# Kernel optimization log

Hardware: AMD Instinct MI355X
Metric: run time of the kernel (lower is better)

The kernel has to match this reference:

```python
import jax, jax.numpy as jnp
import numpy as np

N, B, E = 10000, 4, 160000
C_IN, C_OUT, C_E = 64, 64, 16


def _mk_params(key, c_in, c_out, c_e):
    ks = jax.random.split(key, 8)
    s = 0.1
    return dict(
        w_n=jax.random.normal(ks[0], (c_in, c_out), jnp.float32) * s,
        w_e=jax.random.normal(ks[1], (c_e, c_out), jnp.float32) * s,
        q=jax.random.normal(ks[2], (c_out, c_out), jnp.float32) * s,
        k=jax.random.normal(ks[3], (c_out, c_out), jnp.float32) * s,
        aw=jax.random.normal(ks[4], (3 * c_out, 1), jnp.float32) * s,
        ab=jax.random.normal(ks[5], (1,), jnp.float32) * s,
        ow=jax.random.normal(ks[6], (2 * c_out, c_out), jnp.float32) * s,
        ob=jax.random.normal(ks[7], (c_out,), jnp.float32) * s,
    )


def setup_inputs() -> dict:
    key = jax.random.key(0)
    kx, ke, ka, k1, k2 = jax.random.split(key, 5)
    inp = {
        'X': jax.random.normal(kx, (N, B, C_IN), jnp.float32),
        'edge_index': jax.random.randint(ke, (2, E), 0, N, jnp.int32),
        'edge_attr': jax.random.normal(ka, (E, C_E), jnp.float32),
    }
    p1 = _mk_params(k1, C_IN, C_OUT, C_E)
    p2 = _mk_params(k2, C_OUT, C_OUT, C_E)
    for name, v in p1.items():
        inp[name + '1'] = v
    for name, v in p2.items():
        inp[name + '2'] = v
    return inp


def egnn_conv(x, edge_index, edge_attr, w_n, w_e, q, k, aw, ab, ow, ob, n_nodes):
    # x: [N,B,Cin]; edge_attr: [E,Ce]
    xp = x @ w_n                         # [N,B,C]
    ea = edge_attr @ w_e                 # [E,C]
    src, dst = edge_index[0], edge_index[1]
    xj = xp[src]                         # [E,B,C] gather (source)
    xi = xp[dst]                         # [E,B,C] gather (target)
    qf = xj @ q                          # [E,B,C]
    kf = xi @ k                          # [E,B,C]
    eab = jnp.broadcast_to(ea[:, None, :], qf.shape)  # [E,B,C]
    att_feat = jnp.concatenate([qf, kf, eab], axis=-1)  # [E,B,3C]
    att = jax.nn.sigmoid(att_feat @ aw + ab)            # [E,B,1]
    gate = jax.nn.sigmoid(eab)
    msg = att * xj * gate                # [E,B,C]
    aggr = jax.ops.segment_max(msg, dst, num_segments=n_nodes)  # [N,B,C]
    aggr = jnp.where(jnp.isneginf(aggr), 0.0, aggr)  # empty segments -> 0
    out = jnp.concatenate([xp, aggr], axis=-1) @ ow + ob
    return xp + out


def reference(X, edge_index, edge_attr,
              w_n1, w_e1, q1, k1, aw1, ab1, ow1, ob1,
              w_n2, w_e2, q2, k2, aw2, ab2, ow2, ob2):
    n_nodes = X.shape[0]
    c1 = egnn_conv(X, edge_index, edge_attr, w_n1, w_e1, q1, k1, aw1, ab1, ow1, ob1, n_nodes)
    c1 = jax.nn.leaky_relu(c1, 0.01)
    c2 = egnn_conv(c1, edge_index, edge_attr, w_n2, w_e2, q2, k2, aw2, ab2, ow2, ob2, n_nodes)
    c2 = jax.nn.leaky_relu(c2, 0.01)
    return c2
```

## Files before the change

### kernel.cpp

```cpp
#include <hip/hip_runtime.h>
#include <math.h>

#define NN 10000
#define BB 4
#define EE 160000
#define CC 64
#define CE 16

static constexpr size_t OFF_XPA    = 0;
static constexpr size_t OFF_XPB    = 10240000;
static constexpr size_t OFF_SA     = 20480000;
static constexpr size_t OFF_SB     = 20640000;
static constexpr size_t OFF_VECS   = 20800000;
static constexpr size_t OFF_COUNTS = 20801280;
static constexpr size_t OFF_CURSOR = 20841280;
static constexpr size_t OFF_OFFS   = 20881280;
static constexpr size_t OFF_RECS   = 20921344;
static constexpr size_t OFF_ATT    = 22201344;
static constexpr size_t OFF_SE12   = 24761344;
static constexpr size_t OFF_ORDER  = 26041344;

__device__ __forceinline__ float sigmoidf_(float x) {
    return __builtin_amdgcn_rcpf(1.0f + __expf(-x));
}

__device__ __forceinline__ float bcast_(float v, int l) {
    return __uint_as_float(__builtin_amdgcn_readlane(__float_as_uint(v), l));
}

__global__ void hist_vecs_kernel(const int* __restrict__ ei, int* __restrict__ counts,
                                 const float* __restrict__ q1, const float* __restrict__ k1,
                                 const float* __restrict__ aw1, const float* __restrict__ we1,
                                 const float* __restrict__ q2, const float* __restrict__ k2,
                                 const float* __restrict__ aw2, const float* __restrict__ we2,
                                 float* __restrict__ vecs) {
    int e = blockIdx.x * blockDim.x + threadIdx.x;
    if (e < EE) atomicAdd(&counts[ei[EE + e]], 1);
    if (blockIdx.x == 0) {
        int t = threadIdx.x;
        if (t < 64) {
            float a = 0.f, b = 0.f, c = 0.f, d = 0.f;
            for (int j = 0; j < 64; ++j) {
                a = fmaf(q1[t * 64 + j], aw1[j], a);
                b = fmaf(k1[t * 64 + j], aw1[64 + j], b);
                c = fmaf(q2[t * 64 + j], aw2[j], c);
                d = fmaf(k2[t * 64 + j], aw2[64 + j], d);
            }
            vecs[t] = a; vecs[64 + t] = b; vecs[144 + t] = c; vecs[208 + t] = d;
        }
        if (t < 16) {
            float a = 0.f, b = 0.f;
            for (int j = 0; j < 64; ++j) {
                a = fmaf(we1[t * 64 + j], aw1[128 + j], a);
                b = fmaf(we2[t * 64 + j], aw2[128 + j], b);
            }
            vecs[128 + t] = a; vecs[272 + t] = b;
        }
    }
}

__global__ __launch_bounds__(1024) void scan_order_kernel(const int* __restrict__ counts,
                                                          int* __restrict__ offs,
                                                          int* __restrict__ order) {
    __shared__ int hist[1024];
    __shared__ int cur[1024];
    __shared__ int startb[1024];
    __shared__ int wsum[16];
    int t = threadIdx.x;
    hist[t] = 0; cur[t] = 0;
    int lane = t & 63, wid = t >> 6;
    int v[10];
    int s = 0;
    #pragma unroll
    for (int j = 0; j < 10; ++j) {
        int i = t * 10 + j;
        v[j] = (i < NN) ? counts[i] : 0;
        s += v[j];
    }
    int ps = s;
    #pragma unroll
    for (int off = 1; off < 64; off <<= 1) {
        int u = __shfl_up(ps, off, 64);
        if (lane >= off) ps += u;
    }
    if (lane == 63) wsum[wid] = ps;
    __syncthreads();
    int wbase = 0;
    for (int w = 0; w < wid; ++w) wbase += wsum[w];
    int tb = wbase + ps - s;
    #pragma unroll
    for (int j = 0; j < 10; ++j) {
        int i = t * 10 + j;
        if (i < NN) offs[i] = tb;
        tb += v[j];
    }
    if (t == 1023) offs[NN] = tb;
    #pragma unroll
    for (int j = 0; j < 10; ++j) {
        int i = t * 10 + j;
        if (i < NN) {
            int d = v[j] > 1023 ? 1023 : v[j];
            atomicAdd(&hist[d], 1);
        }
    }
    __syncthreads();
    int r = 1023 - t;
    int hv = hist[r];
    int ps2 = hv;
    #pragma unroll
    for (int off = 1; off < 64; off <<= 1) {
        int u = __shfl_up(ps2, off, 64);
        if (lane >= off) ps2 += u;
    }
    if (lane == 63) wsum[wid] = ps2;
    __syncthreads();
    int wb2 = 0;
    for (int w = 0; w < wid; ++w) wb2 += wsum[w];
    startb[r] = wb2 + ps2 - hv;
    __syncthreads();
    #pragma unroll
    for (int j = 0; j < 10; ++j) {
        int i = t * 10 + j;
        if (i < NN) {
            int d = v[j] > 1023 ? 1023 : v[j];
            int pos = startb[d] + atomicAdd(&cur[d], 1);
            order[pos] = i;
        }
    }
}

__global__ __launch_bounds__(256) void scatter_kernel(
    const int* __restrict__ ei, const int* __restrict__ offs,
    int* __restrict__ cursor, const float* __restrict__ attr,
    const float* __restrict__ vecs, const float* __restrict__ ab1,
    const float* __restrict__ ab2, int2* __restrict__ recs,
    float2* __restrict__ se12) {
    int e = blockIdx.x * blockDim.x + threadIdx.x;
    if (e >= EE) return;
    int s = ei[e], d = ei[EE + e];
    const float4* ap = (const float4*)(attr + (size_t)e * CE);
    float4 a0 = ap[0], a1 = ap[1], a2 = ap[2], a3 = ap[3];
    const float* v1 = vecs + 128;
    const float* v2 = vecs + 272;
    float s1 = ab1[0], s2 = ab2[0];
    s1 = fmaf(a0.x, v1[0], s1);  s1 = fmaf(a0.y, v1[1], s1);
    s1 = fmaf(a0.z, v1[2], s1);  s1 = fmaf(a0.w, v1[3], s1);
    s1 = fmaf(a1.x, v1[4], s1);  s1 = fmaf(a1.y, v1[5], s1);
    s1 = fmaf(a1.z, v1[6], s1);  s1 = fmaf(a1.w, v1[7], s1);
    s1 = fmaf(a2.x, v1[8], s1);  s1 = fmaf(a2.y, v1[9], s1);
    s1 = fmaf(a2.z, v1[10], s1); s1 = fmaf(a2.w, v1[11], s1);
    s1 = fmaf(a3.x, v1[12], s1); s1 = fmaf(a3.y, v1[13], s1);
    s1 = fmaf(a3.z, v1[14], s1); s1 = fmaf(a3.w, v1[15], s1);
    s2 = fmaf(a0.x, v2[0], s2);  s2 = fmaf(a0.y, v2[1], s2);
    s2 = fmaf(a0.z, v2[2], s2);  s2 = fmaf(a0.w, v2[3], s2);
    s2 = fmaf(a1.x, v2[4], s2);  s2 = fmaf(a1.y, v2[5], s2);
    s2 = fmaf(a1.z, v2[6], s2);  s2 = fmaf(a1.w, v2[7], s2);
    s2 = fmaf(a2.x, v2[8], s2);  s2 = fmaf(a2.y, v2[9], s2);
    s2 = fmaf(a2.z, v2[10], s2); s2 = fmaf(a2.w, v2[11], s2);
    s2 = fmaf(a3.x, v2[12], s2); s2 = fmaf(a3.y, v2[13], s2);
    s2 = fmaf(a3.z, v2[14], s2); s2 = fmaf(a3.w, v2[15], s2);
    int p = atomicAdd(&cursor[d], 1);
    recs[offs[d] + p] = make_int2(s, e);
    se12[e] = make_float2(s1, s2);
}

__global__ __launch_bounds__(256) void node_prep_kernel(
    const float* __restrict__ x, const float* __restrict__ w_n,
    const float* __restrict__ qa, const float* __restrict__ ka,
    float* __restrict__ xp, float* __restrict__ sa, float* __restrict__ sb) {
    int t = threadIdx.x, wave = t >> 6, lane = t & 63;
    int node = blockIdx.x * 4 + wave;
    float4 xv = ((const float4*)(x + (size_t)node * BB * CC))[lane];
    float acc0 = 0.f, acc1 = 0.f, acc2 = 0.f, acc3 = 0.f;
    #pragma unroll
    for (int ci = 0; ci < 64; ++ci) {
        float w = w_n[ci * 64 + lane];
        float c0 = ((ci & 3) == 0) ? xv.x : ((ci & 3) == 1) ? xv.y
                 : ((ci & 3) == 2) ? xv.z : xv.w;
        int src = ci >> 2;
        acc0 = fmaf(bcast_(c0, (0 << 4) | src), w, acc0);
        acc1 = fmaf(bcast_(c0, (1 << 4) | src), w, acc1);
        acc2 = fmaf(bcast_(c0, (2 << 4) | src), w, acc2);
        acc3 = fmaf(bcast_(c0, (3 << 4) | src), w, acc3);
    }
    size_t obase = (size_t)node * BB * CC + lane;
    xp[obase] = acc0;
    xp[obase + 64] = acc1;
    xp[obase + 128] = acc2;
    xp[obase + 192] = acc3;
    float qv = qa[lane], kv = ka[lane];
    float ra0 = acc0 * qv, ra1 = acc1 * qv, ra2 = acc2 * qv, ra3 = acc3 * qv;
    float rb0 = acc0 * kv, rb1 = acc1 * kv, rb2 = acc2 * kv, rb3 = acc3 * kv;
    #pragma unroll
    for (int off = 32; off >= 1; off >>= 1) {
        ra0 += __shfl_xor(ra0, off, 64); ra1 += __shfl_xor(ra1, off, 64);
        ra2 += __shfl_xor(ra2, off, 64); ra3 += __shfl_xor(ra3, off, 64);
        rb0 += __shfl_xor(rb0, off, 64); rb1 += __shfl_xor(rb1, off, 64);
        rb2 += __shfl_xor(rb2, off, 64); rb3 += __shfl_xor(rb3, off, 64);
    }
    if (lane == 0) {
        sa[node * BB + 0] = ra0; sa[node * BB + 1] = ra1;
        sa[node * BB + 2] = ra2; sa[node * BB + 3] = ra3;
        sb[node * BB + 0] = rb0; sb[node * BB + 1] = rb1;
        sb[node * BB + 2] = rb2; sb[node * BB + 3] = rb3;
    }
}

__global__ __launch_bounds__(256) void att_kernel(
    const int* __restrict__ ei, const float2* __restrict__ se12,
    const float* __restrict__ sa, const float* __restrict__ sb,
    float4* __restrict__ att, int sel) {
    int e = blockIdx.x * blockDim.x + threadIdx.x;
    if (e >= EE) return;
    int s = ei[e], d = ei[EE + e];
    float2 se2 = se12[e];
    float se = sel ? se2.y : se2.x;
    float4 sas = *(const float4*)(sa + (size_t)s * BB);
    float4 sbn = *(const float4*)(sb + (size_t)d * BB);
    float4 r;
    r.x = sigmoidf_(sas.x + sbn.x + se);
    r.y = sigmoidf_(sas.y + sbn.y + se);
    r.z = sigmoidf_(sas.z + sbn.z + se);
    r.w = sigmoidf_(sas.w + sbn.w + se);
    att[e] = r;
}

__global__ __launch_bounds__(256) void conv_out_kernel(
    const float* __restrict__ xp,
    const int2* __restrict__ recs,
    const int* __restrict__ offs,
    const float* __restrict__ attr,
    const float* __restrict__ w_e,
    const float4* __restrict__ att,
    const float* __restrict__ ow,
    const float* __restrict__ ob,
    const int* __restrict__ order,
    float* __restrict__ out) {
    int t = threadIdx.x;
    int wave = t >> 6, lane = t & 63;
    int node = order[blockIdx.x * 4 + wave];

    float wec[CE];
    #pragma unroll
    for (int j = 0; j < CE; ++j) wec[j] = w_e[j * CC + lane];

    const float* xn = xp + (size_t)node * BB * CC + lane;
    float xn0 = xn[0], xn1 = xn[64], xn2 = xn[128], xn3 = xn[192];

    int o0 = offs[node], o1 = offs[node + 1];
    float m0 = -INFINITY, m1 = -INFINITY, m2 = -INFINITY, m3 = -INFINITY;

    int i = o0;
    int2 rec = (i < o1) ? recs[i] : make_int2(0, 0);
    while (i < o1) {
        int2 cur = rec;
        ++i;
        if (i < o1) rec = recs[i];
        int s = cur.x, e = cur.y;
        float4 at = att[e];
        const float4* ap = (const float4*)(attr + (size_t)e * CE);
        float4 a0 = ap[0], a1 = ap[1], a2 = ap[2], a3 = ap[3];
        float g = 0.f;
        g = fmaf(a0.x, wec[0], g);  g = fmaf(a0.y, wec[1], g);
        g = fmaf(a0.z, wec[2], g);  g = fmaf(a0.w, wec[3], g);
        g = fmaf(a1.x, wec[4], g);  g = fmaf(a1.y, wec[5], g);
        g = fmaf(a1.z, wec[6], g);  g = fmaf(a1.w, wec[7], g);
        g = fmaf(a2.x, wec[8], g);  g = fmaf(a2.y, wec[9], g);
        g = fmaf(a2.z, wec[10], g); g = fmaf(a2.w, wec[11], g);
        g = fmaf(a3.x, wec[12], g); g = fmaf(a3.y, wec[13], g);
        g = fmaf(a3.z, wec[14], g); g = fmaf(a3.w, wec[15], g);
        g = sigmoidf_(g);
        const float* xs = xp + (size_t)s * BB * CC + lane;
        float x0 = xs[0], x1 = xs[64], x2 = xs[128], x3 = xs[192];
        m0 = fmaxf(m0, at.x * x0 * g);
        m1 = fmaxf(m1, at.y * x1 * g);
        m2 = fmaxf(m2, at.z * x2 * g);
        m3 = fmaxf(m3, at.w * x3 * g);
    }
    m0 = (m0 == -INFINITY) ? 0.f : m0;
    m1 = (m1 == -INFINITY) ? 0.f : m1;
    m2 = (m2 == -INFINITY) ? 0.f : m2;
    m3 = (m3 == -INFINITY) ? 0.f : m3;

    float o0f = 0.f, o1f = 0.f, o2f = 0.f, o3f = 0.f;
    #pragma unroll
    for (int ci = 0; ci < 64; ++ci) {
        float wa = ow[ci * 64 + lane];
        float wb = ow[(64 + ci) * 64 + lane];
        o0f = fmaf(bcast_(xn0, ci), wa, o0f);
        o1f = fmaf(bcast_(xn1, ci), wa, o1f);
        o2f = fmaf(bcast_(xn2, ci), wa, o2f);
        o3f = fmaf(bcast_(xn3, ci), wa, o3f);
        o0f = fmaf(bcast_(m0, ci), wb, o0f);
        o1f = fmaf(bcast_(m1, ci), wb, o1f);
        o2f = fmaf(bcast_(m2, ci), wb, o2f);
        o3f = fmaf(bcast_(m3, ci), wb, o3f);
    }
    float obv = ob[lane];
    float r0 = xn0 + o0f + obv;
    float r1 = xn1 + o1f + obv;
    float r2 = xn2 + o2f + obv;
    float r3 = xn3 + o3f + obv;
    r0 = (r0 > 0.f) ? r0 : 0.01f * r0;
    r1 = (r1 > 0.f) ? r1 : 0.01f * r1;
    r2 = (r2 > 0.f) ? r2 : 0.01f * r2;
    r3 = (r3 > 0.f) ? r3 : 0.01f * r3;
    float* op = out + (size_t)node * BB * CC + lane;
    op[0] = r0; op[64] = r1; op[128] = r2; op[192] = r3;
}

extern "C" void kernel_launch(void* const* d_in, const int* in_sizes, int n_in,
                              void* d_out, int out_size, void* d_ws, size_t ws_size,
                              hipStream_t stream) {
    const float* X    = (const float*)d_in[0];
    const int*   ei   = (const int*)d_in[1];
    const float* attr = (const float*)d_in[2];
    const float* w_n1 = (const float*)d_in[3];
    const float* w_e1 = (const float*)d_in[4];
    const float* q1   = (const float*)d_in[5];
    const float* k1   = (const float*)d_in[6];
    const float* aw1  = (const float*)d_in[7];
    const float* ab1  = (const float*)d_in[8];
    const float* ow1  = (const float*)d_in[9];
    const float* ob1  = (const float*)d_in[10];
    const float* w_n2 = (const float*)d_in[11];
    const float* w_e2 = (const float*)d_in[12];
    const float* q2   = (const float*)d_in[13];
    const float* k2   = (const float*)d_in[14];
    const float* aw2  = (const float*)d_in[15];
    const float* ab2  = (const float*)d_in[16];
    const float* ow2  = (const float*)d_in[17];
    const float* ob2  = (const float*)d_in[18];
    float* out = (float*)d_out;

    char* ws = (char*)d_ws;
    float*  xpA    = (float*)(ws + OFF_XPA);
    float*  xpB    = (float*)(ws + OFF_XPB);
    float*  sa     = (float*)(ws + OFF_SA);
    float*  sb     = (float*)(ws + OFF_SB);
    float*  vecs   = (float*)(ws + OFF_VECS);
    int*    counts = (int*)(ws + OFF_COUNTS);
    int*    cursor = (int*)(ws + OFF_CURSOR);
    int*    offs   = (int*)(ws + OFF_OFFS);
    int2*   recs   = (int2*)(ws + OFF_RECS);
    float4* att    = (float4*)(ws + OFF_ATT);
    float2* se12   = (float2*)(ws + OFF_SE12);
    int*    order  = (int*)(ws + OFF_ORDER);

    hipMemsetAsync(counts, 0, 2 * NN * sizeof(int), stream);
    hist_vecs_kernel<<<EE / 256, 256, 0, stream>>>(ei, counts, q1, k1, aw1, w_e1,
                                                   q2, k2, aw2, w_e2, vecs);
    scan_order_kernel<<<1, 1024, 0, stream>>>(counts, offs, order);
    scatter_kernel<<<EE / 256, 256, 0, stream>>>(ei, offs, cursor, attr, vecs,
                                                 ab1, ab2, recs, se12);
    node_prep_kernel<<<NN / 4, 256, 0, stream>>>(X, w_n1, vecs + 0, vecs + 64, xpA, sa, sb);
    att_kernel<<<EE / 256, 256, 0, stream>>>(ei, se12, sa, sb, att, 0);
    conv_out_kernel<<<NN / 4, 256, 0, stream>>>(xpA, recs, offs, attr, w_e1, att,
                                                ow1, ob1, order, xpB);
    node_prep_kernel<<<NN / 4, 256, 0, stream>>>(xpB, w_n2, vecs + 144, vecs + 208, xpA, sa, sb);
    att_kernel<<<EE / 256, 256, 0, stream>>>(ei, se12, sa, sb, att, 1);
    conv_out_kernel<<<NN / 4, 256, 0, stream>>>(xpA, recs, offs, attr, w_e2, att,
                                                ow2, ob2, order, out);
}
```

Baseline: 273.8 us.

## Fuse first-layer attention into scatter and switch intermediates to channel-major float4 layout

Moves the first node_prep launch before the scan so the scatter kernel can compute layer-1 attention directly, removing one att_kernel launch and the se12 round trip (only the layer-2 edge scalar is stored). Intermediate xp buffers are stored batch-interleaved per channel so each lane reads and writes a single float4 instead of four strided scalars, including the per-edge source gather in conv_out. The second node_prep gets a separate loop for the new layout, and the final output keeps the original layout. This adds a layout flag to several kernels and makes the scatter kernel heavier.

```diff
diff --git a/kernel.cpp b/kernel.cpp
--- a/kernel.cpp
+++ b/kernel.cpp
@@ -17,8 +17,9 @@
 static constexpr size_t OFF_OFFS   = 20881280;
 static constexpr size_t OFF_RECS   = 20921344;
 static constexpr size_t OFF_ATT    = 22201344;
-static constexpr size_t OFF_SE12   = 24761344;
-static constexpr size_t OFF_ORDER  = 26041344;
+static constexpr size_t OFF_SE2    = 24761344;
+static constexpr size_t OFF_ORDER  = 25401344;
+
 
 __device__ __forceinline__ float sigmoidf_(float x) {
     return __builtin_amdgcn_rcpf(1.0f + __expf(-x));
@@ -129,12 +130,64 @@
     }
 }
 
+__global__ __launch_bounds__(256) void node_prep_kernel(
+    const float* __restrict__ x, const float* __restrict__ w_n,
+    const float* __restrict__ qa, const float* __restrict__ ka,
+    float* __restrict__ xp, float* __restrict__ sa, float* __restrict__ sb,
+    int in_cm) {
+    int t = threadIdx.x, wave = t >> 6, lane = t & 63;
+    int node = blockIdx.x * 4 + wave;
+    float4 xv = ((const float4*)(x + (size_t)node * BB * CC))[lane];
+    float acc0 = 0.f, acc1 = 0.f, acc2 = 0.f, acc3 = 0.f;
+    if (in_cm) {
+        #pragma unroll
+        for (int ci = 0; ci < 64; ++ci) {
+            float w = w_n[ci * 64 + lane];
+            acc0 = fmaf(bcast_(xv.x, ci), w, acc0);
+            acc1 = fmaf(bcast_(xv.y, ci), w, acc1);
+            acc2 = fmaf(bcast_(xv.z, ci), w, acc2);
+            acc3 = fmaf(bcast_(xv.w, ci), w, acc3);
+        }
+    } else {
+        #pragma unroll
+        for (int ci = 0; ci < 64; ++ci) {
+            float w = w_n[ci * 64 + lane];
+            float c0 = ((ci & 3) == 0) ? xv.x : ((ci & 3) == 1) ? xv.y
+                     : ((ci & 3) == 2) ? xv.z : xv.w;
+            int src = ci >> 2;
+            acc0 = fmaf(bcast_(c0, (0 << 4) | src), w, acc0);
+            acc1 = fmaf(bcast_(c0, (1 << 4) | src), w, acc1);
+            acc2 = fmaf(bcast_(c0, (2 << 4) | src), w, acc2);
+            acc3 = fmaf(bcast_(c0, (3 << 4) | src), w, acc3);
+        }
+    }
+    ((float4*)(xp + (size_t)node * BB * CC))[lane] =
+        make_float4(acc0, acc1, acc2, acc3);
+    float qv = qa[lane], kv = ka[lane];
+    float ra0 = acc0 * qv, ra1 = acc1 * qv, ra2 = acc2 * qv, ra3 = acc3 * qv;
+    float rb0 = acc0 * kv, rb1 = acc1 * kv, rb2 = acc2 * kv, rb3 = acc3 * kv;
+    #pragma unroll
+    for (int off = 32; off >= 1; off >>= 1) {
+        ra0 += __shfl_xor(ra0, off, 64); ra1 += __shfl_xor(ra1, off, 64);
+        ra2 += __shfl_xor(ra2, off, 64); ra3 += __shfl_xor(ra3, off, 64);
+        rb0 += __shfl_xor(rb0, off, 64); rb1 += __shfl_xor(rb1, off, 64);
+        rb2 += __shfl_xor(rb2, off, 64); rb3 += __shfl_xor(rb3, off, 64);
+    }
+    if (lane == 0) {
+        sa[node * BB + 0] = ra0; sa[node * BB + 1] = ra1;
+        sa[node * BB + 2] = ra2; sa[node * BB + 3] = ra3;
+        sb[node * BB + 0] = rb0; sb[node * BB + 1] = rb1;
+        sb[node * BB + 2] = rb2; sb[node * BB + 3] = rb3;
+    }
+}
+
 __global__ __launch_bounds__(256) void scatter_kernel(
     const int* __restrict__ ei, const int* __restrict__ offs,
     int* __restrict__ cursor, const float* __restrict__ attr,
     const float* __restrict__ vecs, const float* __restrict__ ab1,
-    const float* __restrict__ ab2, int2* __restrict__ recs,
-    float2* __restrict__ se12) {
+    const float* __restrict__ ab2, const float* __restrict__ sa,
+    const float* __restrict__ sb, int2* __restrict__ recs,
+    float* __restrict__ se2, float4* __restrict__ att) {
     int e = blockIdx.x * blockDim.x + threadIdx.x;
     if (e >= EE) return;
     int s = ei[e], d = ei[EE + e];
@@ -161,60 +214,25 @@
     s2 = fmaf(a3.z, v2[14], s2); s2 = fmaf(a3.w, v2[15], s2);
     int p = atomicAdd(&cursor[d], 1);
     recs[offs[d] + p] = make_int2(s, e);
-    se12[e] = make_float2(s1, s2);
-}
-
-__global__ __launch_bounds__(256) void node_prep_kernel(
-    const float* __restrict__ x, const float* __restrict__ w_n,
-    const float* __restrict__ qa, const float* __restrict__ ka,
-    float* __restrict__ xp, float* __restrict__ sa, float* __restrict__ sb) {
-    int t = threadIdx.x, wave = t >> 6, lane = t & 63;
-    int node = blockIdx.x * 4 + wave;
-    float4 xv = ((const float4*)(x + (size_t)node * BB * CC))[lane];
-    float acc0 = 0.f, acc1 = 0.f, acc2 = 0.f, acc3 = 0.f;
-    #pragma unroll
-    for (int ci = 0; ci < 64; ++ci) {
-        float w = w_n[ci * 64 + lane];
-        float c0 = ((ci & 3) == 0) ? xv.x : ((ci & 3) == 1) ? xv.y
-                 : ((ci & 3) == 2) ? xv.z : xv.w;
-        int src = ci >> 2;
-        acc0 = fmaf(bcast_(c0, (0 << 4) | src), w, acc0);
-        acc1 = fmaf(bcast_(c0, (1 << 4) | src), w, acc1);
-        acc2 = fmaf(bcast_(c0, (2 << 4) | src), w, acc2);
-        acc3 = fmaf(bcast_(c0, (3 << 4) | src), w, acc3);
-    }
-    size_t obase = (size_t)node * BB * CC + lane;
-    xp[obase] = acc0;
-    xp[obase + 64] = acc1;
-    xp[obase + 128] = acc2;
-    xp[obase + 192] = acc3;
-    float qv = qa[lane], kv = ka[lane];
-    float ra0 = acc0 * qv, ra1 = acc1 * qv, ra2 = acc2 * qv, ra3 = acc3 * qv;
-    float rb0 = acc0 * kv, rb1 = acc1 * kv, rb2 = acc2 * kv, rb3 = acc3 * kv;
-    #pragma unroll
-    for (int off = 32; off >= 1; off >>= 1) {
-        ra0 += __shfl_xor(ra0, off, 64); ra1 += __shfl_xor(ra1, off, 64);
-        ra2 += __shfl_xor(ra2, off, 64); ra3 += __shfl_xor(ra3, off, 64);
-        rb0 += __shfl_xor(rb0, off, 64); rb1 += __shfl_xor(rb1, off, 64);
-        rb2 += __shfl_xor(rb2, off, 64); rb3 += __shfl_xor(rb3, off, 64);
-    }
-    if (lane == 0) {
-        sa[node * BB + 0] = ra0; sa[node * BB + 1] = ra1;
-        sa[node * BB + 2] = ra2; sa[node * BB + 3] = ra3;
-        sb[node * BB + 0] = rb0; sb[node * BB + 1] = rb1;
-        sb[node * BB + 2] = rb2; sb[node * BB + 3] = rb3;
-    }
+    se2[e] = s2;
+    float4 sas = *(const float4*)(sa + (size_t)s * BB);
+    float4 sbn = *(const float4*)(sb + (size_t)d * BB);
+    float4 r;
+    r.x = sigmoidf_(sas.x + sbn.x + s1);
+    r.y = sigmoidf_(sas.y + sbn.y + s1);
+    r.z = sigmoidf_(sas.z + sbn.z + s1);
+    r.w = sigmoidf_(sas.w + sbn.w + s1);
+    att[e] = r;
 }
 
 __global__ __launch_bounds__(256) void att_kernel(
-    const int* __restrict__ ei, const float2* __restrict__ se12,
+    const int* __restrict__ ei, const float* __restrict__ se2,
     const float* __restrict__ sa, const float* __restrict__ sb,
-    float4* __restrict__ att, int sel) {
+    float4* __restrict__ att) {
     int e = blockIdx.x * blockDim.x + threadIdx.x;
     if (e >= EE) return;
     int s = ei[e], d = ei[EE + e];
-    float2 se2 = se12[e];
-    float se = sel ? se2.y : se2.x;
+    float se = se2[e];
     float4 sas = *(const float4*)(sa + (size_t)s * BB);
     float4 sbn = *(const float4*)(sb + (size_t)d * BB);
     float4 r;
@@ -235,7 +253,8 @@
     const float* __restrict__ ow,
     const float* __restrict__ ob,
     const int* __restrict__ order,
-    float* __restrict__ out) {
+    float* __restrict__ out,
+    int out_std) {
     int t = threadIdx.x;
     int wave = t >> 6, lane = t & 63;
     int node = order[blockIdx.x * 4 + wave];
@@ -244,8 +263,8 @@
     #pragma unroll
     for (int j = 0; j < CE; ++j) wec[j] = w_e[j * CC + lane];
 
-    const float* xn = xp + (size_t)node * BB * CC + lane;
-    float xn0 = xn[0], xn1 = xn[64], xn2 = xn[128], xn3 = xn[192];
+    float4 xnv = ((const float4*)(xp + (size_t)node * BB * CC))[lane];
+    float xn0 = xnv.x, xn1 = xnv.y, xn2 = xnv.z, xn3 = xnv.w;
 
     int o0 = offs[node], o1 = offs[node + 1];
     float m0 = -INFINITY, m1 = -INFINITY, m2 = -INFINITY, m3 = -INFINITY;
@@ -270,12 +289,11 @@
         g = fmaf(a3.x, wec[12], g); g = fmaf(a3.y, wec[13], g);
         g = fmaf(a3.z, wec[14], g); g = fmaf(a3.w, wec[15], g);
         g = sigmoidf_(g);
-        const float* xs = xp + (size_t)s * BB * CC + lane;
-        float x0 = xs[0], x1 = xs[64], x2 = xs[128], x3 = xs[192];
-        m0 = fmaxf(m0, at.x * x0 * g);
-        m1 = fmaxf(m1, at.y * x1 * g);
-        m2 = fmaxf(m2, at.z * x2 * g);
-        m3 = fmaxf(m3, at.w * x3 * g);
+        float4 xv4 = ((const float4*)(xp + (size_t)s * BB * CC))[lane];
+        m0 = fmaxf(m0, at.x * xv4.x * g);
+        m1 = fmaxf(m1, at.y * xv4.y * g);
+        m2 = fmaxf(m2, at.z * xv4.z * g);
+        m3 = fmaxf(m3, at.w * xv4.w * g);
     }
     m0 = (m0 == -INFINITY) ? 0.f : m0;
     m1 = (m1 == -INFINITY) ? 0.f : m1;
@@ -305,8 +323,13 @@
     r1 = (r1 > 0.f) ? r1 : 0.01f * r1;
     r2 = (r2 > 0.f) ? r2 : 0.01f * r2;
     r3 = (r3 > 0.f) ? r3 : 0.01f * r3;
-    float* op = out + (size_t)node * BB * CC + lane;
-    op[0] = r0; op[64] = r1; op[128] = r2; op[192] = r3;
+    if (out_std) {
+        float* op = out + (size_t)node * BB * CC + lane;
+        op[0] = r0; op[64] = r1; op[128] = r2; op[192] = r3;
+    } else {
+        ((float4*)(out + (size_t)node * BB * CC))[lane] =
+            make_float4(r0, r1, r2, r3);
+    }
 }
 
 extern "C" void kernel_launch(void* const* d_in, const int* in_sizes, int n_in,
@@ -344,21 +367,22 @@
     int*    offs   = (int*)(ws + OFF_OFFS);
     int2*   recs   = (int2*)(ws + OFF_RECS);
     float4* att    = (float4*)(ws + OFF_ATT);
-    float2* se12   = (float2*)(ws + OFF_SE12);
+    float*  se2    = (float*)(ws + OFF_SE2);
     int*    order  = (int*)(ws + OFF_ORDER);
 
     hipMemsetAsync(counts, 0, 2 * NN * sizeof(int), stream);
     hist_vecs_kernel<<<EE / 256, 256, 0, stream>>>(ei, counts, q1, k1, aw1, w_e1,
                                                    q2, k2, aw2, w_e2, vecs);
+    node_prep_kernel<<<NN / 4, 256, 0, stream>>>(X, w_n1, vecs + 0, vecs + 64,
+                                                 xpA, sa, sb, 0);
     scan_order_kernel<<<1, 1024, 0, stream>>>(counts, offs, order);
     scatter_kernel<<<EE / 256, 256, 0, stream>>>(ei, offs, cursor, attr, vecs,
-                                                 ab1, ab2, recs, se12);
-    node_prep_kernel<<<NN / 4, 256, 0, stream>>>(X, w_n1, vecs + 0, vecs + 64, xpA, sa, sb);
-    att_kernel<<<EE / 256, 256, 0, stream>>>(ei, se12, sa, sb, att, 0);
+                                                 ab1, ab2, sa, sb, recs, se2, att);
     conv_out_kernel<<<NN / 4, 256, 0, stream>>>(xpA, recs, offs, attr, w_e1, att,
-                                                ow1, ob1, order, xpB);
-    node_prep_kernel<<<NN / 4, 256, 0, stream>>>(xpB, w_n2, vecs + 144, vecs + 208, xpA, sa, sb);
-    att_kernel<<<EE / 256, 256, 0, stream>>>(ei, se12, sa, sb, att, 1);
+                                                ow1, ob1, order, xpB, 0);
+    node_prep_kernel<<<NN / 4, 256, 0, stream>>>(xpB, w_n2, vecs + 144, vecs + 208,
+                                                 xpA, sa, sb, 1);
+    att_kernel<<<EE / 256, 256, 0, stream>>>(ei, se2, sa, sb, att);
     conv_out_kernel<<<NN / 4, 256, 0, stream>>>(xpA, recs, offs, attr, w_e2, att,
-                                                ow2, ob2, order, out);
-}
+                                                ow2, ob2, order, out, 1);
+}
```

Result: no change. 270.9 us (-1.1%).
